# Optimization experiments

Hardware: AMD Instinct MI355X
Metric: run time of the kernel (lower is better)

The kernel has to match this reference:

```python
import jax, jax.numpy as jnp
import numpy as np

N = 50000          # nodes
E = 800000         # edges (before self-loops)
F_IN = 128         # num_features
HEADS = 4
OUT = 128 // HEADS # per-head channels = num_hidden // heads
NEG_SLOPE = 0.2    # PyG GATConv default


def setup_inputs() -> dict:
    key = jax.random.key(0)
    ks = jax.random.split(key, 10)
    x = jax.random.normal(ks[0], (N, F_IN), jnp.float32)
    edge_index = jax.random.randint(ks[1], (2, E), 0, N, dtype=jnp.int64)
    sW = 1.0 / np.sqrt(F_IN)
    sA = 1.0 / np.sqrt(OUT)
    return {
        "x": x,
        "edge_index": edge_index,
        "W1": jax.random.normal(ks[2], (F_IN, HEADS * OUT), jnp.float32) * sW,
        "a_src1": jax.random.normal(ks[3], (HEADS, OUT), jnp.float32) * sA,
        "a_dst1": jax.random.normal(ks[4], (HEADS, OUT), jnp.float32) * sA,
        "b1": jnp.zeros((HEADS * OUT,), jnp.float32),
        "W2": jax.random.normal(ks[5], (HEADS * OUT, HEADS * OUT), jnp.float32) * sW,
        "a_src2": jax.random.normal(ks[6], (HEADS, OUT), jnp.float32) * sA,
        "a_dst2": jax.random.normal(ks[7], (HEADS, OUT), jnp.float32) * sA,
        "b2": jnp.zeros((HEADS * OUT,), jnp.float32),
    }


def gat_conv(x, src, dst, W, a_src, a_dst, b):
    """One GATConv layer (PyG semantics, concat heads, self-loops already in src/dst)."""
    n = x.shape[0]
    h = (x @ W).reshape(n, HEADS, OUT)                 # [N, H, C]
    # per-node attention halves, gathered per edge -> [Etot, H]
    alpha = (h * a_src).sum(-1)[src] + (h * a_dst).sum(-1)[dst]
    alpha = jax.nn.leaky_relu(alpha, NEG_SLOPE)
    # softmax over incoming edges of each destination node (stable)
    amax = jax.ops.segment_max(alpha, dst, num_segments=n)
    ex = jnp.exp(alpha - amax[dst])
    denom = jax.ops.segment_sum(ex, dst, num_segments=n)
    attn = ex / (denom[dst] + 1e-16)                    # [Etot, H]
    # weighted message scatter-add
    out = jax.ops.segment_sum(h[src] * attn[..., None], dst, num_segments=n)
    return out.reshape(n, HEADS * OUT) + b


def reference(x, edge_index, W1, a_src1, a_dst1, b1, W2, a_src2, a_dst2, b2):
    loops = jnp.arange(N, dtype=edge_index.dtype)       # PyG add_self_loops=True
    src = jnp.concatenate([edge_index[0], loops])
    dst = jnp.concatenate([edge_index[1], loops])
    h = jax.nn.relu(gat_conv(x, src, dst, W1, a_src1, a_dst1, b1))
    # dropout = identity in eval mode
    h = jax.nn.relu(gat_conv(h, src, dst, W2, a_src2, a_dst2, b2))
    return h
```

## Files before the change

kernel.cpp:

```cpp
#include <hip/hip_runtime.h>
#include <hip/hip_fp16.h>
#include <cstdint>
#include <cstddef>

#define NN 50000
#define EE 800000
#define ETOT (EE + NN)
#define FD 128
#define NH 4
#define NEG_SLOPE 0.2f

#define BSHIFT 10
#define BSIZE 1024
#define NBKT ((NN + BSIZE - 1) / BSIZE)
#define CAPG 20000
#define CHUNK 2048
#define P1_BLOCKS ((ETOT + CHUNK - 1) / CHUNK)
#define GEMM_BLOCKS ((NN + 63) / 64)
#define ADOT_BLOCKS ((NN * 16 + 1023) / 1024)

typedef _Float16 half8 __attribute__((ext_vector_type(8)));
typedef float f32x4 __attribute__((ext_vector_type(4)));


__device__ __forceinline__ void gemm_body(const float* __restrict__ X,
                                          const uint4* __restrict__ Wf,
                                          __half* __restrict__ Hh,
                                          int bidx, int tid) {
    const int wv = tid >> 6, lane = tid & 63;
    const int l15 = lane & 15, lg = lane >> 4;
    const int rowA = bidx * 64 + wv * 16 + l15;
    const int rA = (rowA < NN) ? rowA : NN - 1;
    half8 a[4];
    #pragma unroll
    for (int ks = 0; ks < 4; ++ks) {
        int kb = ks * 32 + lg * 8;
        float4 x0 = *(const float4*)&X[(size_t)rA * FD + kb];
        float4 x1 = *(const float4*)&X[(size_t)rA * FD + kb + 4];
        a[ks][0] = (_Float16)x0.x; a[ks][1] = (_Float16)x0.y;
        a[ks][2] = (_Float16)x0.z; a[ks][3] = (_Float16)x0.w;
        a[ks][4] = (_Float16)x1.x; a[ks][5] = (_Float16)x1.y;
        a[ks][6] = (_Float16)x1.z; a[ks][7] = (_Float16)x1.w;
    }
    const int rowC = bidx * 64 + wv * 16 + lg * 4;
    #pragma unroll
    for (int ct = 0; ct < 8; ++ct) {
        uint4 braw[4];
        #pragma unroll
        for (int ks = 0; ks < 4; ++ks) braw[ks] = Wf[(ct * 4 + ks) * 64 + lane];
        f32x4 acc = {0.f, 0.f, 0.f, 0.f};
        #pragma unroll
        for (int ks = 0; ks < 4; ++ks) {
            half8 b = *(half8*)&braw[ks];
            acc = __builtin_amdgcn_mfma_f32_16x16x32_f16(a[ks], b, acc, 0, 0, 0);
        }
        #pragma unroll
        for (int r = 0; r < 4; ++r) {
            int gr = rowC + r;
            if (gr < NN) Hh[(size_t)gr * FD + ct * 16 + l15] = __float2half(acc[r]);
        }
    }
}

__device__ __forceinline__ void adot_body(const __half* __restrict__ H,
                                          const float* __restrict__ a_src,
                                          const float* __restrict__ a_dst,
                                          float* __restrict__ AS,
                                          float* __restrict__ AD, int gt) {
    int n = gt >> 4;
    int l = gt & 15;
    if (n >= NN) return;
    union { uint4 u; __half2 q[4]; } hv;
    hv.u = *(const uint4*)&H[(size_t)n * FD + l * 8];
    float ps = 0.f, pd = 0.f;
    #pragma unroll
    for (int j = 0; j < 4; ++j) {
        float2 f = __half22float2(hv.q[j]);
        ps += f.x * a_src[l * 8 + 2 * j] + f.y * a_src[l * 8 + 2 * j + 1];
        pd += f.x * a_dst[l * 8 + 2 * j] + f.y * a_dst[l * 8 + 2 * j + 1];
    }
    ps += __shfl_xor(ps, 1); ps += __shfl_xor(ps, 2);
    pd += __shfl_xor(pd, 1); pd += __shfl_xor(pd, 2);
    if ((l & 3) == 0) {
        AS[n * NH + (l >> 2)] = ps;
        AD[n * NH + (l >> 2)] = pd;
    }
}


__global__ __launch_bounds__(256) void init_kernel(int* __restrict__ gcnt,
                                                   const float* __restrict__ W1,
                                                   const float* __restrict__ W2,
                                                   uint4* __restrict__ Wf1,
                                                   uint4* __restrict__ Wf2) {
    if (blockIdx.x == 0) {
        if (threadIdx.x < NBKT) gcnt[threadIdx.x] = 0;
        return;
    }
    const float* W = (blockIdx.x == 2) ? W2 : W1;
    uint4* Wf = (blockIdx.x == 2) ? Wf2 : Wf1;
    for (int s = threadIdx.x; s < 2048; s += 256) {
        int fi = s >> 6;
        int lane = s & 63;
        int ct = fi >> 2, ks = fi & 3;
        int col = ct * 16 + (lane & 15);
        int kb = ks * 32 + (lane >> 4) * 8;
        half8 h;
        #pragma unroll
        for (int j = 0; j < 8; ++j) h[j] = (_Float16)W[(kb + j) * FD + col];
        Wf[s] = *(uint4*)&h;
    }
}


__global__ __launch_bounds__(256) void binGemm_kernel(const int* __restrict__ ei,
                                                      int* __restrict__ gcnt,
                                                      uint32_t* __restrict__ gbkt,
                                                      const float* __restrict__ X,
                                                      const uint4* __restrict__ Wf1,
                                                      __half* __restrict__ Hh) {
    if (blockIdx.x >= P1_BLOCKS) {
        gemm_body(X, Wf1, Hh, blockIdx.x - P1_BLOCKS, threadIdx.x);
        return;
    }
    __shared__ int lcnt[NBKT];
    __shared__ int gb[NBKT];
    const int t = threadIdx.x;
    if (t < NBKT) lcnt[t] = 0;
    __syncthreads();
    const int base = blockIdx.x * CHUNK;
    uint32_t pk[8]; int bk[8]; int sl[8];
    #pragma unroll
    for (int j = 0; j < 8; ++j) {
        int e = base + j * 256 + t;
        bk[j] = -1;
        if (e < ETOT) {
            int src, dst;
            if (e < EE) { src = ei[e]; dst = ei[EE + e]; }
            else        { src = e - EE; dst = src; }
            int b = dst >> BSHIFT;
            bk[j] = b;
            pk[j] = (uint32_t)src | ((uint32_t)(dst & (BSIZE - 1)) << 16);
            sl[j] = atomicAdd(&lcnt[b], 1);
        }
    }
    __syncthreads();
    if (t < NBKT) gb[t] = atomicAdd(&gcnt[t], lcnt[t]);
    __syncthreads();
    #pragma unroll
    for (int j = 0; j < 8; ++j)
        if (bk[j] >= 0)
            gbkt[(size_t)bk[j] * CAPG + gb[bk[j]] + sl[j]] = pk[j];
}


__global__ __launch_bounds__(1024) void sortAdot_kernel(const int* __restrict__ gcnt,
                                                        const uint32_t* __restrict__ gbkt,
                                                        int* __restrict__ row_ptr,
                                                        int* __restrict__ csr,
                                                        const __half* __restrict__ Hh,
                                                        const float* __restrict__ a_src,
                                                        const float* __restrict__ a_dst,
                                                        float* __restrict__ AS,
                                                        float* __restrict__ AD) {
    if (blockIdx.x >= NBKT) {
        adot_body(Hh, a_src, a_dst, AS, AD,
                  (blockIdx.x - NBKT) * 1024 + threadIdx.x);
        return;
    }
    __shared__ int cnt[BSIZE];
    __shared__ int pfx[BSIZE];
    __shared__ int wsum[16];
    __shared__ int sCbase;
    const int b = blockIdx.x;
    const int t = threadIdx.x;
    const int count = gcnt[b];
    const int dstBase = b << BSHIFT;
    const int ndst = (NN - dstBase < BSIZE) ? (NN - dstBase) : BSIZE;
    const uint32_t* mybkt = gbkt + (size_t)b * CAPG;
    cnt[t] = 0;
    if (t < 64) {
        int v = (t < NBKT) ? gcnt[t] : 0;
        int inc = v;
        #pragma unroll
        for (int off = 1; off < 64; off <<= 1) {
            int u = __shfl_up(inc, off);
            if (t >= off) inc += u;
        }
        if (t == b) sCbase = inc - v;
    }
    __syncthreads();
    const int cbase = sCbase;
    for (int i = t; i < count; i += 1024)
        atomicAdd(&cnt[mybkt[i] >> 16], 1);
    __syncthreads();
    int v = cnt[t];
    int inc = v;
    const int lane = t & 63, wid = t >> 6;
    #pragma unroll
    for (int off = 1; off < 64; off <<= 1) {
        int u = __shfl_up(inc, off);
        if (lane >= off) inc += u;
    }
    if (lane == 63) wsum[wid] = inc;
    __syncthreads();
    if (t < 16) {
        int w = wsum[t]; int wi = w;
        #pragma unroll
        for (int off = 1; off < 16; off <<= 1) {
            int u = __shfl_up(wi, off);
            if (t >= off) wi += u;
        }
        wsum[t] = wi - w;
    }
    __syncthreads();
    int excl = wsum[wid] + inc - v;
    pfx[t] = excl;
    if (t < ndst) row_ptr[dstBase + t] = cbase + excl;
    if (b == NBKT - 1 && t == 0) row_ptr[NN] = ETOT;
    cnt[t] = 0;
    __syncthreads();
    for (int i = t; i < count; i += 1024) {
        uint32_t pkv = mybkt[i];
        int dl = pkv >> 16;
        int r = atomicAdd(&cnt[dl], 1);
        csr[cbase + pfx[dl] + r] = (int)(pkv & 0xFFFFu);
    }
}


__global__ __launch_bounds__(256) void gemm_kernel(const float* __restrict__ X,
                                                   const uint4* __restrict__ Wf,
                                                   __half* __restrict__ Hh) {
    gemm_body(X, Wf, Hh, blockIdx.x, threadIdx.x);
}

__global__ __launch_bounds__(256) void adot_kernel(const __half* __restrict__ H,
                                                   const float* __restrict__ a_src,
                                                   const float* __restrict__ a_dst,
                                                   float* __restrict__ AS,
                                                   float* __restrict__ AD) {
    adot_body(H, a_src, a_dst, AS, AD, blockIdx.x * 256 + threadIdx.x);
}


__global__ __launch_bounds__(256) void agg_kernel(const __half* __restrict__ H,
                                                  const float* __restrict__ AS,
                                                  const float* __restrict__ AD,
                                                  const int* __restrict__ row_ptr,
                                                  const int* __restrict__ csr_src,
                                                  const float* __restrict__ bias,
                                                  float* __restrict__ Out) {
    __shared__ float sP[8][32][4];
    __shared__ int   sS[8][32];
    const int wave = threadIdx.x >> 6;
    const int lane = threadIdx.x & 63;
    const int sub  = lane >> 5;
    const int sl   = lane & 31;
    const int ws   = wave * 2 + sub;
    const int n = blockIdx.x * 8 + ws;
    const int start = row_ptr[n], end = row_ptr[n + 1];
    const int h0 = sl >> 3;
    const float4 adv = *(const float4*)&AD[n * NH];
    float spm = 0.f;
    float acc0 = 0.f, acc1 = 0.f, acc2 = 0.f, acc3 = 0.f;

    for (int base = start; base < end; base += 32) {
        int cn = end - base; if (cn > 32) cn = 32;
        int my_src = 0;
        float al[NH] = {0.f, 0.f, 0.f, 0.f};
        if (sl < cn) {
            my_src = csr_src[base + sl];
            float4 asv = *(const float4*)&AS[my_src * NH];
            al[0] = asv.x + adv.x; al[1] = asv.y + adv.y;
            al[2] = asv.z + adv.z; al[3] = asv.w + adv.w;
        }
        sS[ws][sl] = my_src;
        float4 pv;
        {
            float a0 = (al[0] > 0.f) ? al[0] : NEG_SLOPE * al[0];
            float a1 = (al[1] > 0.f) ? al[1] : NEG_SLOPE * al[1];
            float a2 = (al[2] > 0.f) ? al[2] : NEG_SLOPE * al[2];
            float a3 = (al[3] > 0.f) ? al[3] : NEG_SLOPE * al[3];
            pv.x = __expf(a0); pv.y = __expf(a1);
            pv.z = __expf(a2); pv.w = __expf(a3);
        }
        *(float4*)&sP[ws][sl][0] = pv;
        #pragma unroll 4
        for (int e = 0; e < cn; ++e) {
            float pm = sP[ws][e][h0];
            int se = sS[ws][e];
            union { uint2 u; __half2 q[2]; } hv;
            hv.u = *(const uint2*)&H[(size_t)se * FD + sl * 4];
            float2 f0 = __half22float2(hv.q[0]);
            float2 f1 = __half22float2(hv.q[1]);
            acc0 += pm * f0.x; acc1 += pm * f0.y;
            acc2 += pm * f1.x; acc3 += pm * f1.y;
            spm  += pm;
        }
    }
    float inv = 1.f / (spm + 1e-16f);
    const float4 bv = *(const float4*)&bias[sl * 4];
    float4 ov;
    ov.x = fmaxf(acc0 * inv + bv.x, 0.f);
    ov.y = fmaxf(acc1 * inv + bv.y, 0.f);
    ov.z = fmaxf(acc2 * inv + bv.z, 0.f);
    ov.w = fmaxf(acc3 * inv + bv.w, 0.f);
    *(float4*)&Out[(size_t)n * FD + sl * 4] = ov;
}


extern "C" void kernel_launch(void* const* d_in, const int* in_sizes, int n_in,
                              void* d_out, int out_size, void* d_ws, size_t ws_size,
                              hipStream_t stream) {
    const float* x     = (const float*)d_in[0];
    const int*   ei    = (const int*)d_in[1];
    const float* W1    = (const float*)d_in[2];
    const float* asrc1 = (const float*)d_in[3];
    const float* adst1 = (const float*)d_in[4];
    const float* b1    = (const float*)d_in[5];
    const float* W2    = (const float*)d_in[6];
    const float* asrc2 = (const float*)d_in[7];
    const float* adst2 = (const float*)d_in[8];
    const float* b2    = (const float*)d_in[9];
    float* out = (float*)d_out;

    char* p = (char*)d_ws;
    auto alloc = [&](size_t bytes) {
        char* q = p;
        p += (bytes + 255) & ~(size_t)255;
        return q;
    };
    int*      row_ptr = (int*)alloc((NN + 1) * sizeof(int));
    int*      gcnt    = (int*)alloc(NBKT * sizeof(int));
    uint32_t* gbkt    = (uint32_t*)alloc((size_t)NBKT * CAPG * sizeof(uint32_t));
    int*      csr     = (int*)alloc((size_t)ETOT * sizeof(int));
    float*    AS      = (float*)alloc((size_t)NN * NH * sizeof(float));
    float*    AD      = (float*)alloc((size_t)NN * NH * sizeof(float));
    __half*   Hh      = (__half*)alloc((size_t)NN * FD * sizeof(__half));
    uint4*    Wf1     = (uint4*)alloc(2048 * sizeof(uint4));
    uint4*    Wf2     = (uint4*)alloc(2048 * sizeof(uint4));
    (void)ws_size; (void)in_sizes; (void)n_in; (void)out_size;

    init_kernel<<<3, 256, 0, stream>>>(gcnt, W1, W2, Wf1, Wf2);
    binGemm_kernel<<<P1_BLOCKS + GEMM_BLOCKS, 256, 0, stream>>>(ei, gcnt, gbkt, x, Wf1, Hh);
    sortAdot_kernel<<<NBKT + ADOT_BLOCKS, 1024, 0, stream>>>(gcnt, gbkt, row_ptr, csr,
                                                             Hh, asrc1, adst1, AS, AD);
    agg_kernel<<<NN / 8, 256, 0, stream>>>(Hh, AS, AD, row_ptr, csr, b1, out);
    gemm_kernel<<<GEMM_BLOCKS, 256, 0, stream>>>(out, Wf2, Hh);
    adot_kernel<<<(NN * 16 + 255) / 256, 256, 0, stream>>>(Hh, asrc2, adst2, AS, AD);
    agg_kernel<<<NN / 8, 256, 0, stream>>>(Hh, AS, AD, row_ptr, csr, b2, out);
}
```

Measured before the change: 133.6 us.

## Precompute W·a attention vectors so adot runs on input X alongside GEMM

```diff
diff --git a/kernel.cpp b/kernel.cpp
--- a/kernel.cpp
+++ b/kernel.cpp
@@ -17,7 +17,7 @@
 #define CHUNK 2048
 #define P1_BLOCKS ((ETOT + CHUNK - 1) / CHUNK)
 #define GEMM_BLOCKS ((NN + 63) / 64)
-#define ADOT_BLOCKS ((NN * 16 + 1023) / 1024)
+#define ADOTX_BLOCKS ((NN * 16 + 255) / 256)
 
 typedef _Float16 half8 __attribute__((ext_vector_type(8)));
 typedef float f32x4 __attribute__((ext_vector_type(4)));
@@ -62,28 +62,33 @@
     }
 }
 
-__device__ __forceinline__ void adot_body(const __half* __restrict__ H,
-                                          const float* __restrict__ a_src,
-                                          const float* __restrict__ a_dst,
-                                          float* __restrict__ AS,
-                                          float* __restrict__ AD, int gt) {
+__device__ __forceinline__ void adotx_body(const float* __restrict__ X,
+                                           const float* __restrict__ WA,
+                                           float* __restrict__ AS,
+                                           float* __restrict__ AD, int gt) {
     int n = gt >> 4;
     int l = gt & 15;
     if (n >= NN) return;
-    union { uint4 u; __half2 q[4]; } hv;
-    hv.u = *(const uint4*)&H[(size_t)n * FD + l * 8];
-    float ps = 0.f, pd = 0.f;
-    #pragma unroll
-    for (int j = 0; j < 4; ++j) {
-        float2 f = __half22float2(hv.q[j]);
-        ps += f.x * a_src[l * 8 + 2 * j] + f.y * a_src[l * 8 + 2 * j + 1];
-        pd += f.x * a_dst[l * 8 + 2 * j] + f.y * a_dst[l * 8 + 2 * j + 1];
-    }
-    ps += __shfl_xor(ps, 1); ps += __shfl_xor(ps, 2);
-    pd += __shfl_xor(pd, 1); pd += __shfl_xor(pd, 2);
-    if ((l & 3) == 0) {
-        AS[n * NH + (l >> 2)] = ps;
-        AD[n * NH + (l >> 2)] = pd;
+    float4 v0 = *(const float4*)&X[(size_t)n * FD + l * 8];
+    float4 v1 = *(const float4*)&X[(size_t)n * FD + l * 8 + 4];
+    float xv[8] = {v0.x, v0.y, v0.z, v0.w, v1.x, v1.y, v1.z, v1.w};
+    float p[8] = {};
+    #pragma unroll
+    for (int j = 0; j < 8; ++j) {
+        const float4 w0 = *(const float4*)&WA[(l * 8 + j) * 8];
+        const float4 w1 = *(const float4*)&WA[(l * 8 + j) * 8 + 4];
+        p[0] += xv[j] * w0.x; p[1] += xv[j] * w0.y;
+        p[2] += xv[j] * w0.z; p[3] += xv[j] * w0.w;
+        p[4] += xv[j] * w1.x; p[5] += xv[j] * w1.y;
+        p[6] += xv[j] * w1.z; p[7] += xv[j] * w1.w;
+    }
+    #pragma unroll
+    for (int m = 1; m <= 8; m <<= 1)
+        #pragma unroll
+        for (int o = 0; o < 8; ++o) p[o] += __shfl_xor(p[o], m);
+    if (l == 0) {
+        *(float4*)&AS[n * NH] = make_float4(p[0], p[1], p[2], p[3]);
+        *(float4*)&AD[n * NH] = make_float4(p[4], p[5], p[6], p[7]);
     }
 }
 
@@ -92,23 +97,46 @@
                                                    const float* __restrict__ W1,
                                                    const float* __restrict__ W2,
                                                    uint4* __restrict__ Wf1,
-                                                   uint4* __restrict__ Wf2) {
+                                                   uint4* __restrict__ Wf2,
+                                                   const float* __restrict__ asrc1,
+                                                   const float* __restrict__ adst1,
+                                                   const float* __restrict__ asrc2,
+                                                   const float* __restrict__ adst2,
+                                                   float* __restrict__ WA1,
+                                                   float* __restrict__ WA2) {
     if (blockIdx.x == 0) {
         if (threadIdx.x < NBKT) gcnt[threadIdx.x] = 0;
         return;
     }
-    const float* W = (blockIdx.x == 2) ? W2 : W1;
-    uint4* Wf = (blockIdx.x == 2) ? Wf2 : Wf1;
-    for (int s = threadIdx.x; s < 2048; s += 256) {
-        int fi = s >> 6;
-        int lane = s & 63;
-        int ct = fi >> 2, ks = fi & 3;
-        int col = ct * 16 + (lane & 15);
-        int kb = ks * 32 + (lane >> 4) * 8;
-        half8 h;
-        #pragma unroll
-        for (int j = 0; j < 8; ++j) h[j] = (_Float16)W[(kb + j) * FD + col];
-        Wf[s] = *(uint4*)&h;
+    if (blockIdx.x <= 2) {
+        const float* W = (blockIdx.x == 2) ? W2 : W1;
+        uint4* Wf = (blockIdx.x == 2) ? Wf2 : Wf1;
+        for (int s = threadIdx.x; s < 2048; s += 256) {
+            int fi = s >> 6;
+            int lane = s & 63;
+            int ct = fi >> 2, ks = fi & 3;
+            int col = ct * 16 + (lane & 15);
+            int kb = ks * 32 + (lane >> 4) * 8;
+            half8 h;
+            #pragma unroll
+            for (int j = 0; j < 8; ++j) h[j] = (_Float16)W[(kb + j) * FD + col];
+            Wf[s] = *(uint4*)&h;
+        }
+        return;
+    }
+    const float* W  = (blockIdx.x == 4) ? W2 : W1;
+    const float* as = (blockIdx.x == 4) ? asrc2 : asrc1;
+    const float* ad = (blockIdx.x == 4) ? adst2 : adst1;
+    float* WA = (blockIdx.x == 4) ? WA2 : WA1;
+    for (int idx = threadIdx.x; idx < 1024; idx += 256) {
+        int k = idx >> 3, o = idx & 7;
+        int h = o & 3;
+        const float* a = (o < 4) ? as : ad;
+        float s = 0.f;
+        #pragma unroll 8
+        for (int j = 0; j < 32; ++j)
+            s += W[k * FD + h * 32 + j] * a[h * 32 + j];
+        WA[k * 8 + o] = s;
     }
 }
 
@@ -118,7 +146,15 @@
                                                       uint32_t* __restrict__ gbkt,
                                                       const float* __restrict__ X,
                                                       const uint4* __restrict__ Wf1,
-                                                      __half* __restrict__ Hh) {
+                                                      __half* __restrict__ Hh,
+                                                      const float* __restrict__ WA1,
+                                                      float* __restrict__ AS,
+                                                      float* __restrict__ AD) {
+    if (blockIdx.x >= P1_BLOCKS + GEMM_BLOCKS) {
+        adotx_body(X, WA1, AS, AD,
+                   (blockIdx.x - P1_BLOCKS - GEMM_BLOCKS) * 256 + threadIdx.x);
+        return;
+    }
     if (blockIdx.x >= P1_BLOCKS) {
         gemm_body(X, Wf1, Hh, blockIdx.x - P1_BLOCKS, threadIdx.x);
         return;
@@ -154,20 +190,10 @@
 }
 
 
-__global__ __launch_bounds__(1024) void sortAdot_kernel(const int* __restrict__ gcnt,
-                                                        const uint32_t* __restrict__ gbkt,
-                                                        int* __restrict__ row_ptr,
-                                                        int* __restrict__ csr,
-                                                        const __half* __restrict__ Hh,
-                                                        const float* __restrict__ a_src,
-                                                        const float* __restrict__ a_dst,
-                                                        float* __restrict__ AS,
-                                                        float* __restrict__ AD) {
-    if (blockIdx.x >= NBKT) {
-        adot_body(Hh, a_src, a_dst, AS, AD,
-                  (blockIdx.x - NBKT) * 1024 + threadIdx.x);
-        return;
-    }
+__global__ __launch_bounds__(1024) void sort_kernel(const int* __restrict__ gcnt,
+                                                    const uint32_t* __restrict__ gbkt,
+                                                    int* __restrict__ row_ptr,
+                                                    int* __restrict__ csr) {
     __shared__ int cnt[BSIZE];
     __shared__ int pfx[BSIZE];
     __shared__ int wsum[16];
@@ -229,18 +255,17 @@
 }
 
 
-__global__ __launch_bounds__(256) void gemm_kernel(const float* __restrict__ X,
-                                                   const uint4* __restrict__ Wf,
-                                                   __half* __restrict__ Hh) {
+__global__ __launch_bounds__(256) void gemmAdot_kernel(const float* __restrict__ X,
+                                                       const uint4* __restrict__ Wf,
+                                                       __half* __restrict__ Hh,
+                                                       const float* __restrict__ WA,
+                                                       float* __restrict__ AS,
+                                                       float* __restrict__ AD) {
+    if (blockIdx.x >= GEMM_BLOCKS) {
+        adotx_body(X, WA, AS, AD, (blockIdx.x - GEMM_BLOCKS) * 256 + threadIdx.x);
+        return;
+    }
     gemm_body(X, Wf, Hh, blockIdx.x, threadIdx.x);
-}
-
-__global__ __launch_bounds__(256) void adot_kernel(const __half* __restrict__ H,
-                                                   const float* __restrict__ a_src,
-                                                   const float* __restrict__ a_dst,
-                                                   float* __restrict__ AS,
-                                                   float* __restrict__ AD) {
-    adot_body(H, a_src, a_dst, AS, AD, blockIdx.x * 256 + threadIdx.x);
 }
 
 
@@ -340,14 +365,17 @@
     __half*   Hh      = (__half*)alloc((size_t)NN * FD * sizeof(__half));
     uint4*    Wf1     = (uint4*)alloc(2048 * sizeof(uint4));
     uint4*    Wf2     = (uint4*)alloc(2048 * sizeof(uint4));
+    float*    WA1     = (float*)alloc(1024 * sizeof(float));
+    float*    WA2     = (float*)alloc(1024 * sizeof(float));
     (void)ws_size; (void)in_sizes; (void)n_in; (void)out_size;
 
-    init_kernel<<<3, 256, 0, stream>>>(gcnt, W1, W2, Wf1, Wf2);
-    binGemm_kernel<<<P1_BLOCKS + GEMM_BLOCKS, 256, 0, stream>>>(ei, gcnt, gbkt, x, Wf1, Hh);
-    sortAdot_kernel<<<NBKT + ADOT_BLOCKS, 1024, 0, stream>>>(gcnt, gbkt, row_ptr, csr,
-                                                             Hh, asrc1, adst1, AS, AD);
+    init_kernel<<<5, 256, 0, stream>>>(gcnt, W1, W2, Wf1, Wf2,
+                                       asrc1, adst1, asrc2, adst2, WA1, WA2);
+    binGemm_kernel<<<P1_BLOCKS + GEMM_BLOCKS + ADOTX_BLOCKS, 256, 0, stream>>>(
+        ei, gcnt, gbkt, x, Wf1, Hh, WA1, AS, AD);
+    sort_kernel<<<NBKT, 1024, 0, stream>>>(gcnt, gbkt, row_ptr, csr);
     agg_kernel<<<NN / 8, 256, 0, stream>>>(Hh, AS, AD, row_ptr, csr, b1, out);
-    gemm_kernel<<<GEMM_BLOCKS, 256, 0, stream>>>(out, Wf2, Hh);
-    adot_kernel<<<(NN * 16 + 255) / 256, 256, 0, stream>>>(Hh, asrc2, adst2, AS, AD);
+    gemmAdot_kernel<<<GEMM_BLOCKS + ADOTX_BLOCKS, 256, 0, stream>>>(
+        out, Wf2, Hh, WA2, AS, AD);
     agg_kernel<<<NN / 8, 256, 0, stream>>>(Hh, AS, AD, row_ptr, csr, b2, out);
 }
```

New measurement: 173.9 us. 1.3x slower.
